# Performance work log

Measured on AMD Instinct MI355X. Metric: run time of the kernel, lower is better.

The kernel has to match this reference:

```python
import jax, jax.numpy as jnp
import numpy as np

B, T, D, I, C, H = 8192, 128, 7, 128, 10, 64
L = 2 ** D
SUBSET = int(I * 0.8)  # feature_subset_size = 102


def setup_inputs() -> dict:
    key = jax.random.key(0)
    ks = jax.random.split(key, 7)
    x = jax.random.normal(ks[0], (B, I), dtype=jnp.float32)
    # exact feature-subset mask: SUBSET ones per (tree, depth) row
    r = jax.random.uniform(ks[1], (T, D, I))
    ranks = jnp.argsort(jnp.argsort(r, axis=-1), axis=-1)
    feature_mask = (ranks < SUBSET).astype(jnp.float32)
    thresholds = jax.random.normal(ks[2], (T, D), dtype=jnp.float32)
    leaf_outputs = jax.random.normal(ks[3], (T, L, C), dtype=jnp.float32)
    W1 = jax.random.normal(ks[4], (I, H), dtype=jnp.float32) * 0.08
    b1 = jnp.zeros((H,), dtype=jnp.float32)
    W2 = jax.random.normal(ks[5], (H, T), dtype=jnp.float32) * 0.12
    b2 = jnp.zeros((T,), dtype=jnp.float32)
    return {"x": x, "feature_mask": feature_mask, "thresholds": thresholds,
            "leaf_outputs": leaf_outputs, "W1": W1, "b1": b1, "W2": W2, "b2": b2}


def reference(x, feature_mask, thresholds, leaf_outputs, W1, b1, W2, b2):
    depth = thresholds.shape[1]
    # split logits: masked feature sum minus threshold, per (batch, tree, depth)
    z = jnp.einsum('bi,tdi->btd', x, feature_mask) - thresholds[None, :, :]
    s = 0.5 * (z / (1.0 + jnp.abs(z)) + 1.0)  # scaled softsign split in (0,1)
    # probabilistic path routing: doubling concat, identical to torch loop
    p = jnp.ones((x.shape[0], feature_mask.shape[0], 1), dtype=x.dtype)
    for d in range(depth):
        sd = s[:, :, d:d + 1]            # [B, T, 1]
        p = jnp.concatenate([p * sd, p * (1.0 - sd)], axis=-1)  # [B, T, 2^(d+1)]
    leaf_probs = jax.nn.softmax(leaf_outputs, axis=-1)           # [T, L, C]
    tree_outputs = jnp.einsum('btl,tlc->btc', p, leaf_probs)     # [B, T, C]
    # instance-wise attention over trees (eval mode: no dropout)
    attn = jax.nn.softmax(jax.nn.relu(x @ W1 + b1) @ W2 + b2, axis=-1)  # [B, T]
    return jnp.sum(tree_outputs * attn[:, :, None], axis=1)     # [B, C]
```

## Files before the change

kernel.cpp:

```cpp
#include <hip/hip_runtime.h>
#include <hip/hip_bf16.h>
#include <hip/hip_fp16.h>


#define BB 8192
#define TT 128
#define II 128
#define CC 10
#define HH 64

#define OFF_LPB 524288
#define OFF_XBF 606208
#define OFF_MBF 1130496

typedef __attribute__((ext_vector_type(8))) short short8;
typedef __attribute__((ext_vector_type(16))) float floatx16;

static __device__ inline unsigned int pkbf(float lo, float hi) {
  __hip_bfloat162 h = __float22bfloat162_rn(make_float2(lo, hi));
  unsigned int u;
  __builtin_memcpy(&u, &h, 4);
  return u;
}

static __device__ inline unsigned int pkh(float lo, float hi) {
  __half2 h = __float22half2_rn(make_float2(lo, hi));
  unsigned int u;
  __builtin_memcpy(&u, &h, 4);
  return u;
}

static __device__ inline short8 cvt8(float4 a, float4 b) {
  union { short8 v; unsigned int u[4]; } r;
  r.u[0] = pkbf(a.x, a.y);
  r.u[1] = pkbf(a.z, a.w);
  r.u[2] = pkbf(b.x, b.y);
  r.u[3] = pkbf(b.z, b.w);
  return r.v;
}

__global__ __launch_bounds__(64) void prep_kernel(
    const float* __restrict__ x, const float* __restrict__ mask,
    const float* __restrict__ lo,
    const float* __restrict__ W1, const float* __restrict__ b1,
    const float* __restrict__ W2, const float* __restrict__ b2,
    __half* __restrict__ attnB, unsigned int* __restrict__ lpbG,
    unsigned short* __restrict__ xbf, unsigned short* __restrict__ mbf,
    float* __restrict__ out) {
  __shared__ __align__(16) char smem_raw[6144];
  const int blk = blockIdx.x;
  const int lane = threadIdx.x;
  const int half = lane >> 5, l31 = lane & 31;

  if (blk < 256) {
    const int b0 = blk * 32;

    short8 axf[8];
    const float* xrow = x + (size_t)(b0 + l31) * II + half * 8;
#pragma unroll
    for (int s = 0; s < 8; ++s)
      axf[s] = cvt8(*(const float4*)(xrow + s * 16),
                    *(const float4*)(xrow + s * 16 + 4));

    floatx16 acch[2];
#pragma unroll
    for (int i = 0; i < 16; ++i) { acch[0][i] = 0.f; acch[1][i] = 0.f; }
#pragma unroll
    for (int s = 0; s < 8; ++s) {
#pragma unroll
      for (int tile = 0; tile < 2; ++tile) {
        union { short8 v; unsigned int u[4]; } wf;
#pragma unroll
        for (int jp = 0; jp < 4; ++jp) {
          int k0 = s * 16 + half * 8 + jp * 2;
          float f0 = W1[(size_t)k0 * HH + tile * 32 + l31];
          float f1 = W1[(size_t)(k0 + 1) * HH + tile * 32 + l31];
          wf.u[jp] = pkbf(f0, f1);
        }
        acch[tile] = __builtin_amdgcn_mfma_f32_32x32x16_bf16(
            axf[s], wf.v, acch[tile], 0, 0, 0);
      }
    }
    __hip_bfloat16* hids = (__hip_bfloat16*)smem_raw;
#pragma unroll
    for (int tile = 0; tile < 2; ++tile) {
      float bh = b1[tile * 32 + l31];
#pragma unroll
      for (int r = 0; r < 16; ++r) {
        int row = (r & 3) + 8 * (r >> 2) + 4 * half;
        hids[row * 72 + tile * 32 + l31] =
            __float2bfloat16(fmaxf(acch[tile][r] + bh, 0.f));
      }
    }
    __syncthreads();

    short8 ahf[4];
#pragma unroll
    for (int s = 0; s < 4; ++s)
      ahf[s] = *(const short8*)(hids + l31 * 72 + s * 16 + half * 8);

    floatx16 accl[4];
#pragma unroll
    for (int tile = 0; tile < 4; ++tile) {
#pragma unroll
      for (int i = 0; i < 16; ++i) accl[tile][i] = 0.f;
#pragma unroll
      for (int s = 0; s < 4; ++s) {
        union { short8 v; unsigned int u[4]; } wf;
#pragma unroll
        for (int jp = 0; jp < 4; ++jp) {
          int k0 = s * 16 + half * 8 + jp * 2;
          float f0 = W2[(size_t)k0 * TT + tile * 32 + l31];
          float f1 = W2[(size_t)(k0 + 1) * TT + tile * 32 + l31];
          wf.u[jp] = pkbf(f0, f1);
        }
        accl[tile] = __builtin_amdgcn_mfma_f32_32x32x16_bf16(
            ahf[s], wf.v, accl[tile], 0, 0, 0);
      }
      float bt = b2[tile * 32 + l31];
#pragma unroll
      for (int i = 0; i < 16; ++i) accl[tile][i] += bt;
    }

    float mrow[16];
#pragma unroll
    for (int r = 0; r < 16; ++r)
      mrow[r] = fmaxf(fmaxf(accl[0][r], accl[1][r]),
                      fmaxf(accl[2][r], accl[3][r]));
#pragma unroll
    for (int msk = 1; msk <= 16; msk <<= 1)
#pragma unroll
      for (int r = 0; r < 16; ++r)
        mrow[r] = fmaxf(mrow[r], __shfl_xor(mrow[r], msk, 64));
    float srow[16];
#pragma unroll
    for (int r = 0; r < 16; ++r) srow[r] = 0.f;
#pragma unroll
    for (int tile = 0; tile < 4; ++tile)
#pragma unroll
      for (int r = 0; r < 16; ++r) {
        float e = __expf(accl[tile][r] - mrow[r]);
        accl[tile][r] = e;
        srow[r] += e;
      }
#pragma unroll
    for (int msk = 1; msk <= 16; msk <<= 1)
#pragma unroll
      for (int r = 0; r < 16; ++r)
        srow[r] += __shfl_xor(srow[r], msk, 64);
#pragma unroll
    for (int r = 0; r < 16; ++r) srow[r] = 1.f / srow[r];

#pragma unroll
    for (int tile = 0; tile < 4; ++tile)
#pragma unroll
      for (int r = 0; r < 16; ++r) {
        int row = (r & 3) + 8 * (r >> 2) + 4 * half;
        attnB[(size_t)(b0 + row) * TT + tile * 32 + l31] =
            __float2half(accl[tile][r] * srow[r]);
      }

  } else if (blk < 384) {
    float* lps = (float*)smem_raw;
    const int t0 = blk - 256;
#pragma unroll
    for (int rr = 0; rr < 2; ++rr) {
      int l = lane * 2 + rr;
      const float* row = lo + ((size_t)t0 * 128 + l) * CC;
      float v[CC];
      float m = -1e30f;
#pragma unroll
      for (int c = 0; c < CC; ++c) { v[c] = row[c]; m = fmaxf(m, v[c]); }
      float s = 0.f;
#pragma unroll
      for (int c = 0; c < CC; ++c) { v[c] = __expf(v[c] - m); s += v[c]; }
      float inv = 1.f / s;
      float* o = lps + l * 12;
#pragma unroll
      for (int c = 0; c < CC; ++c) o[c] = v[c] * inv;
    }
    __syncthreads();

#pragma unroll
    for (int jj = 0; jj < 3; ++jj) {
      int idx = jj * 64 + lane;
      if (idx < 160) {
        int s = idx / 20, e = idx - s * 20;
        int n = e >> 1, hf = e & 1;
        unsigned int wd[4];
#pragma unroll
        for (int jp = 0; jp < 4; ++jp) {
          int l0 = s * 16 + hf * 8 + jp * 2;
          float f0 = lps[l0 * 12 + n];
          float f1 = lps[(l0 + 1) * 12 + n];
          wd[jp] = pkh(f0, f1);
        }
        ((uint4*)lpbG)[(size_t)t0 * 160 + idx] =
            make_uint4(wd[0], wd[1], wd[2], wd[3]);
      }
    }
  } else if (blk < 668) {
    const float* src;
    unsigned short* dst;
    size_t base;
    if (blk < 640) { src = x;    dst = xbf; base = (size_t)(blk - 384) * 4096; }
    else           { src = mask; dst = mbf; base = (size_t)(blk - 640) * 4096; }
#pragma unroll
    for (int j = 0; j < 8; ++j) {
      size_t e = base + (size_t)j * 512 + (size_t)lane * 8;
      float4 a = *(const float4*)(src + e);
      float4 b = *(const float4*)(src + e + 4);
      *(short8*)(dst + e) = cvt8(a, b);
    }
  } else {
    const int base4 = (blk - 668) * 512;
#pragma unroll
    for (int j = 0; j < 8; ++j)
      ((float4*)out)[base4 + j * 64 + lane] = make_float4(0.f, 0.f, 0.f, 0.f);
  }
}

__global__ __launch_bounds__(256, 4) void main_kernel(
    const unsigned short* __restrict__ xbf, const unsigned short* __restrict__ mbf,
    const float* __restrict__ thr, const __half* __restrict__ attnB,
    const unsigned int* __restrict__ lpbG, float* __restrict__ out) {
  __shared__ __align__(16) char smem_raw[16384];
  const int tid = threadIdx.x;
  const int wv = tid >> 6, lane = tid & 63;
  const int half = lane >> 5, l31 = lane & 31;
  const int phys = blockIdx.x;
  const int bg2 = (phys & 7) + ((phys >> 7) << 3);
  const int tg  = (phys >> 3) & 15;
  const int bl = wv * 32 + l31;

  __half* zsl = (__half*)smem_raw;

  __half av[8];
  *(uint4*)av = ((const uint4*)attnB)[(size_t)(bg2 * 128 + bl) * 16 + tg];

  {
    const int m0 = tg * 56;
    short8 xf[8];
    const unsigned short* xr = xbf + (size_t)(bg2 * 128 + bl) * II + half * 8;
#pragma unroll
    for (int s = 0; s < 8; ++s) xf[s] = *(const short8*)(xr + s * 16);

#pragma unroll
    for (int tile = 0; tile < 2; ++tile) {
      int mr = m0 + tile * 28 + l31; if (mr > 895) mr = 895;
      const unsigned short* mrow = mbf + (size_t)mr * II + half * 8;
      short8 af[8];
#pragma unroll
      for (int s = 0; s < 8; ++s) af[s] = *(const short8*)(mrow + s * 16);
      float th[16];
#pragma unroll
      for (int r = 0; r < 16; ++r) {
        int row = (r & 3) + 8 * (r >> 2) + 4 * half;
        int mrr = m0 + tile * 28 + row;
        th[r] = thr[mrr > 895 ? 895 : mrr];
      }
      floatx16 acc;
#pragma unroll
      for (int i = 0; i < 16; ++i) acc[i] = 0.f;
#pragma unroll
      for (int s = 0; s < 8; ++s)
        acc = __builtin_amdgcn_mfma_f32_32x32x16_bf16(af[s], xf[s], acc, 0, 0, 0);

#pragma unroll
      for (int r = 0; r < 16; ++r) {
        int row = (r & 3) + 8 * (r >> 2) + 4 * half;
        if (row < 28) {
          int tl = row / 7;
          int d = row - tl * 7;
          float z = acc[r] - th[r];
          float o = 0.5f * (z / (1.f + fabsf(z)) + 1.f);
          zsl[((tl + tile * 4) * 128 + bl) * 8 + d] = __float2half(o);
        }
      }
    }
  }

  {
    const uint4* zsl4 = (const uint4*)smem_raw;
    const uint4* lpt = (const uint4*)lpbG + (size_t)tg * 1280;

    floatx16 acc;
#pragma unroll
    for (int i = 0; i < 16; ++i) acc[i] = 0.f;

    auto dostep = [&](int it, const uint4* bf) {
      uint4 sv = zsl4[it * 128 + bl];
      const __half* sh = (const __half*)&sv;
      float s0 = __half2float(sh[0]), s1 = __half2float(sh[1]);
      float s2 = __half2float(sh[2]), s3 = __half2float(sh[3]);
      float s4 = __half2float(sh[4]), s5 = __half2float(sh[5]);
      float s6 = __half2float(sh[6]);
      float A  = __half2float(av[it]);

      float s0c = 1.f - s0, s1c = 1.f - s1, s2c = 1.f - s2;
      float t0 = s0 * s1, t1 = s0c * s1, t2 = s0 * s1c, t3 = s0c * s1c;
      float pl[8];
      pl[0] = t0 * s2;  pl[1] = t1 * s2;  pl[2] = t2 * s2;  pl[3] = t3 * s2;
      pl[4] = t0 * s2c; pl[5] = t1 * s2c; pl[6] = t2 * s2c; pl[7] = t3 * s2c;
      float sel3 = half ? (1.f - s3) : s3;
      float Af = A * sel3;
      float s4c = 1.f - s4, s5c = 1.f - s5;
      float as6 = Af * s6, as6c = Af * (1.f - s6);
      float u0 = s4 * s5, u1 = s4c * s5, u2 = s4 * s5c, u3 = s4c * s5c;
      float wv8[8];
      wv8[0] = u0 * as6;  wv8[1] = u1 * as6;
      wv8[2] = u2 * as6;  wv8[3] = u3 * as6;
      wv8[4] = u0 * as6c; wv8[5] = u1 * as6c;
      wv8[6] = u2 * as6c; wv8[7] = u3 * as6c;
      __half2 pl2[4];
#pragma unroll
      for (int jp = 0; jp < 4; ++jp)
        pl2[jp] = __float22half2_rn(make_float2(pl[jp * 2], pl[jp * 2 + 1]));

#pragma unroll
      for (int s = 0; s < 8; ++s) {
        union { short8 v; __half2 h[4]; } a0;
        __half2 w2 = __half2half2(__float2half(wv8[s]));
#pragma unroll
        for (int jp = 0; jp < 4; ++jp) a0.h[jp] = __hmul2(pl2[jp], w2);
        acc = __builtin_amdgcn_mfma_f32_32x32x16_f16(
            a0.v, *(const short8*)&bf[s], acc, 0, 0, 0);
      }
    };

#define PF(dst, itn)                                                       \
  _Pragma("unroll") for (int s = 0; s < 8; ++s)                            \
      dst[s] = (l31 < CC) ? lpt[((itn) * 8 + s) * 20 + l31 * 2 + half]     \
                          : make_uint4(0u, 0u, 0u, 0u);

    uint4 bf0[8], bf1[8];
    PF(bf0, 0)
#pragma unroll
    for (int ith = 0; ith < 4; ++ith) {
      const int it = ith * 2;
      PF(bf1, it + 1)
      dostep(it, bf0);
      if (ith < 3) { PF(bf0, it + 2) }
      dostep(it + 1, bf1);
    }
#undef PF

    __syncthreads();
    float* red = (float*)smem_raw;
    if (l31 < CC) {
#pragma unroll
      for (int r = 0; r < 16; ++r) {
        int row = (r & 3) + 8 * (r >> 2) + 4 * half;
        red[(wv * 32 + row) * 10 + l31] = acc[r];
      }
    }
    __syncthreads();
#pragma unroll
    for (int j = 0; j < 5; ++j) {
      int idx = tid + 256 * j;
      atomicAdd(out + (size_t)bg2 * 1280 + idx, red[idx]);
    }
  }
}

extern "C" void kernel_launch(void* const* d_in, const int* in_sizes, int n_in,
                              void* d_out, int out_size, void* d_ws, size_t ws_size,
                              hipStream_t stream) {
  const float* x    = (const float*)d_in[0];
  const float* mask = (const float*)d_in[1];
  const float* thr  = (const float*)d_in[2];
  const float* lo   = (const float*)d_in[3];
  const float* W1   = (const float*)d_in[4];
  const float* b1   = (const float*)d_in[5];
  const float* W2   = (const float*)d_in[6];
  const float* b2   = (const float*)d_in[7];
  float* out = (float*)d_out;
  float* ws  = (float*)d_ws;

  __half*         attnB = (__half*)ws;
  unsigned int*   LPb   = (unsigned int*)(ws + OFF_LPB);
  unsigned short* xbf   = (unsigned short*)(ws + OFF_XBF);
  unsigned short* mbf   = (unsigned short*)(ws + OFF_MBF);

  prep_kernel<<<708, 64, 0, stream>>>(x, mask, lo, W1, b1, W2, b2,
                                      attnB, LPb, xbf, mbf, out);
  main_kernel<<<1024, 256, 0, stream>>>(xbf, mbf, thr, attnB, LPb, out);
}
```

Measured before the change: 101.7 us.

## Halve trees per block, stage leaf probs in LDS, double grid size

```diff
diff --git a/kernel.cpp b/kernel.cpp
--- a/kernel.cpp
+++ b/kernel.cpp
@@ -220,76 +220,84 @@
   }
 }
 
-__global__ __launch_bounds__(256, 4) void main_kernel(
+__global__ __launch_bounds__(256, 6) void main_kernel(
     const unsigned short* __restrict__ xbf, const unsigned short* __restrict__ mbf,
     const float* __restrict__ thr, const __half* __restrict__ attnB,
     const unsigned int* __restrict__ lpbG, float* __restrict__ out) {
-  __shared__ __align__(16) char smem_raw[16384];
+  __shared__ __align__(16) char smem_raw[18432];
   const int tid = threadIdx.x;
   const int wv = tid >> 6, lane = tid & 63;
   const int half = lane >> 5, l31 = lane & 31;
   const int phys = blockIdx.x;
-  const int bg2 = (phys & 7) + ((phys >> 7) << 3);
-  const int tg  = (phys >> 3) & 15;
+  const int bg2 = (phys & 7) * 8 + (phys >> 8);
+  const int tg4 = (phys >> 3) & 31;
   const int bl = wv * 32 + l31;
 
   __half* zsl = (__half*)smem_raw;
-
-  __half av[8];
-  *(uint4*)av = ((const uint4*)attnB)[(size_t)(bg2 * 128 + bl) * 16 + tg];
+  uint4* st4 = (uint4*)(smem_raw + 8192);
+
+  const uint4* lpg = (const uint4*)lpbG + (size_t)tg4 * 640;
+  uint4 stg0 = lpg[wv * 64 + lane];
+  uint4 stg1 = lpg[(wv + 4) * 64 + lane];
+  uint4 stg2 = make_uint4(0u, 0u, 0u, 0u);
+  if (wv < 2) stg2 = lpg[(wv + 8) * 64 + lane];
+
+  __half av[4];
+  *(uint2*)av = ((const uint2*)attnB)[(size_t)(bg2 * 128 + bl) * 32 + tg4];
 
   {
-    const int m0 = tg * 56;
+    const int m0 = tg4 * 28;
     short8 xf[8];
     const unsigned short* xr = xbf + (size_t)(bg2 * 128 + bl) * II + half * 8;
 #pragma unroll
     for (int s = 0; s < 8; ++s) xf[s] = *(const short8*)(xr + s * 16);
 
-#pragma unroll
-    for (int tile = 0; tile < 2; ++tile) {
-      int mr = m0 + tile * 28 + l31; if (mr > 895) mr = 895;
-      const unsigned short* mrow = mbf + (size_t)mr * II + half * 8;
-      short8 af[8];
-#pragma unroll
-      for (int s = 0; s < 8; ++s) af[s] = *(const short8*)(mrow + s * 16);
-      float th[16];
-#pragma unroll
-      for (int r = 0; r < 16; ++r) {
-        int row = (r & 3) + 8 * (r >> 2) + 4 * half;
-        int mrr = m0 + tile * 28 + row;
-        th[r] = thr[mrr > 895 ? 895 : mrr];
-      }
-      floatx16 acc;
-#pragma unroll
-      for (int i = 0; i < 16; ++i) acc[i] = 0.f;
-#pragma unroll
-      for (int s = 0; s < 8; ++s)
-        acc = __builtin_amdgcn_mfma_f32_32x32x16_bf16(af[s], xf[s], acc, 0, 0, 0);
-
-#pragma unroll
-      for (int r = 0; r < 16; ++r) {
-        int row = (r & 3) + 8 * (r >> 2) + 4 * half;
-        if (row < 28) {
-          int tl = row / 7;
-          int d = row - tl * 7;
-          float z = acc[r] - th[r];
-          float o = 0.5f * (z / (1.f + fabsf(z)) + 1.f);
-          zsl[((tl + tile * 4) * 128 + bl) * 8 + d] = __float2half(o);
-        }
+    int mr = m0 + l31; if (mr > 895) mr = 895;
+    const unsigned short* mrow = mbf + (size_t)mr * II + half * 8;
+
+    floatx16 acc;
+#pragma unroll
+    for (int i = 0; i < 16; ++i) acc[i] = 0.f;
+#pragma unroll
+    for (int s = 0; s < 8; ++s) {
+      short8 af = *(const short8*)(mrow + s * 16);
+      acc = __builtin_amdgcn_mfma_f32_32x32x16_bf16(af, xf[s], acc, 0, 0, 0);
+    }
+
+#pragma unroll
+    for (int r = 0; r < 16; ++r) {
+      int row = (r & 3) + 8 * (r >> 2) + 4 * half;
+      if (row < 28) {
+        int tl = row / 7;
+        int d = row - tl * 7;
+        float z = acc[r] - thr[m0 + row];
+        float o = 0.5f * (z / (1.f + fabsf(z)) + 1.f);
+        zsl[((tl * 128) + bl) * 8 + d] = __float2half(o);
       }
     }
   }
+
+  st4[wv * 64 + lane] = stg0;
+  st4[(wv + 4) * 64 + lane] = stg1;
+  if (wv < 2) st4[(wv + 8) * 64 + lane] = stg2;
+  __syncthreads();
 
   {
     const uint4* zsl4 = (const uint4*)smem_raw;
-    const uint4* lpt = (const uint4*)lpbG + (size_t)tg * 1280;
 
     floatx16 acc;
 #pragma unroll
     for (int i = 0; i < 16; ++i) acc[i] = 0.f;
 
-    auto dostep = [&](int it, const uint4* bf) {
+#pragma unroll
+    for (int it = 0; it < 4; ++it) {
+      uint4 bf[8];
+#pragma unroll
+      for (int s = 0; s < 8; ++s)
+        bf[s] = (l31 < CC) ? st4[(it * 8 + s) * 20 + l31 * 2 + half]
+                           : make_uint4(0u, 0u, 0u, 0u);
       uint4 sv = zsl4[it * 128 + bl];
+
       const __half* sh = (const __half*)&sv;
       float s0 = __half2float(sh[0]), s1 = __half2float(sh[1]);
       float s2 = __half2float(sh[2]), s3 = __half2float(sh[3]);
@@ -326,24 +334,7 @@
         acc = __builtin_amdgcn_mfma_f32_32x32x16_f16(
             a0.v, *(const short8*)&bf[s], acc, 0, 0, 0);
       }
-    };
-
-#define PF(dst, itn)                                                       \
-  _Pragma("unroll") for (int s = 0; s < 8; ++s)                            \
-      dst[s] = (l31 < CC) ? lpt[((itn) * 8 + s) * 20 + l31 * 2 + half]     \
-                          : make_uint4(0u, 0u, 0u, 0u);
-
-    uint4 bf0[8], bf1[8];
-    PF(bf0, 0)
-#pragma unroll
-    for (int ith = 0; ith < 4; ++ith) {
-      const int it = ith * 2;
-      PF(bf1, it + 1)
-      dostep(it, bf0);
-      if (ith < 3) { PF(bf0, it + 2) }
-      dostep(it + 1, bf1);
-    }
-#undef PF
+    }
 
     __syncthreads();
     float* red = (float*)smem_raw;
@@ -384,5 +375,5 @@
 
   prep_kernel<<<708, 64, 0, stream>>>(x, mask, lo, W1, b1, W2, b2,
                                       attnB, LPb, xbf, mbf, out);
-  main_kernel<<<1024, 256, 0, stream>>>(xbf, mbf, thr, attnB, LPb, out);
-}
+  main_kernel<<<2048, 256, 0, stream>>>(xbf, mbf, thr, attnB, LPb, out);
+}
```

After: 106.7 us. 1.05x slower.

## Keep split probabilities in registers via cross-half shuffles instead of LDS staging

Applied to the files above, without the earlier changes.

```diff
diff --git a/kernel.cpp b/kernel.cpp
--- a/kernel.cpp
+++ b/kernel.cpp
@@ -224,7 +224,7 @@
     const unsigned short* __restrict__ xbf, const unsigned short* __restrict__ mbf,
     const float* __restrict__ thr, const __half* __restrict__ attnB,
     const unsigned int* __restrict__ lpbG, float* __restrict__ out) {
-  __shared__ __align__(16) char smem_raw[16384];
+  __shared__ __align__(16) float red[1280];
   const int tid = threadIdx.x;
   const int wv = tid >> 6, lane = tid & 63;
   const int half = lane >> 5, l31 = lane & 31;
@@ -233,11 +233,10 @@
   const int tg  = (phys >> 3) & 15;
   const int bl = wv * 32 + l31;
 
-  __half* zsl = (__half*)smem_raw;
-
   __half av[8];
   *(uint4*)av = ((const uint4*)attnB)[(size_t)(bg2 * 128 + bl) * 16 + tg];
 
+  uint4 sv[8];
   {
     const int m0 = tg * 56;
     short8 xf[8];
@@ -249,53 +248,59 @@
     for (int tile = 0; tile < 2; ++tile) {
       int mr = m0 + tile * 28 + l31; if (mr > 895) mr = 895;
       const unsigned short* mrow = mbf + (size_t)mr * II + half * 8;
-      short8 af[8];
-#pragma unroll
-      for (int s = 0; s < 8; ++s) af[s] = *(const short8*)(mrow + s * 16);
-      float th[16];
+
+      floatx16 acc;
+#pragma unroll
+      for (int i = 0; i < 16; ++i) acc[i] = 0.f;
+#pragma unroll
+      for (int s = 0; s < 8; ++s) {
+        short8 af = *(const short8*)(mrow + s * 16);
+        acc = __builtin_amdgcn_mfma_f32_32x32x16_bf16(af, xf[s], acc, 0, 0, 0);
+      }
+
+      float o[16], po[16];
 #pragma unroll
       for (int r = 0; r < 16; ++r) {
         int row = (r & 3) + 8 * (r >> 2) + 4 * half;
         int mrr = m0 + tile * 28 + row;
-        th[r] = thr[mrr > 895 ? 895 : mrr];
-      }
-      floatx16 acc;
-#pragma unroll
-      for (int i = 0; i < 16; ++i) acc[i] = 0.f;
-#pragma unroll
-      for (int s = 0; s < 8; ++s)
-        acc = __builtin_amdgcn_mfma_f32_32x32x16_bf16(af[s], xf[s], acc, 0, 0, 0);
-
-#pragma unroll
-      for (int r = 0; r < 16; ++r) {
-        int row = (r & 3) + 8 * (r >> 2) + 4 * half;
-        if (row < 28) {
-          int tl = row / 7;
-          int d = row - tl * 7;
-          float z = acc[r] - th[r];
-          float o = 0.5f * (z / (1.f + fabsf(z)) + 1.f);
-          zsl[((tl + tile * 4) * 128 + bl) * 8 + d] = __float2half(o);
-        }
-      }
+        float th = thr[mrr > 895 ? 895 : mrr];
+        float z = acc[r] - th;
+        o[r] = 0.5f * (z / (1.f + fabsf(z)) + 1.f);
+      }
+#pragma unroll
+      for (int r = 0; r < 16; ++r) po[r] = __shfl_xor(o[r], 32, 64);
+      float lo16[16], hi16[16];
+#pragma unroll
+      for (int r = 0; r < 16; ++r) {
+        lo16[r] = half ? po[r] : o[r];
+        hi16[r] = half ? o[r] : po[r];
+      }
+#define OA(rw) (((((rw) >> 2) & 1) ? hi16 : lo16)[((rw) & 3) + (((rw) >> 3) << 2)])
+#pragma unroll
+      for (int tl = 0; tl < 4; ++tl) {
+        sv[tile * 4 + tl] = make_uint4(
+            pkh(OA(7 * tl + 0), OA(7 * tl + 1)),
+            pkh(OA(7 * tl + 2), OA(7 * tl + 3)),
+            pkh(OA(7 * tl + 4), OA(7 * tl + 5)),
+            pkh(OA(7 * tl + 6), OA(7 * tl + 6)));
+      }
+#undef OA
     }
   }
 
   {
-    const uint4* zsl4 = (const uint4*)smem_raw;
     const uint4* lpt = (const uint4*)lpbG + (size_t)tg * 1280;
 
     floatx16 acc;
 #pragma unroll
     for (int i = 0; i < 16; ++i) acc[i] = 0.f;
 
-    auto dostep = [&](int it, const uint4* bf) {
-      uint4 sv = zsl4[it * 128 + bl];
-      const __half* sh = (const __half*)&sv;
+    auto dostep = [&](int it, const uint4* bf, uint4 svv, float A) {
+      const __half* sh = (const __half*)&svv;
       float s0 = __half2float(sh[0]), s1 = __half2float(sh[1]);
       float s2 = __half2float(sh[2]), s3 = __half2float(sh[3]);
       float s4 = __half2float(sh[4]), s5 = __half2float(sh[5]);
       float s6 = __half2float(sh[6]);
-      float A  = __half2float(av[it]);
 
       float s0c = 1.f - s0, s1c = 1.f - s1, s2c = 1.f - s2;
       float t0 = s0 * s1, t1 = s0c * s1, t2 = s0 * s1c, t3 = s0c * s1c;
@@ -339,14 +344,12 @@
     for (int ith = 0; ith < 4; ++ith) {
       const int it = ith * 2;
       PF(bf1, it + 1)
-      dostep(it, bf0);
+      dostep(it, bf0, sv[it], __half2float(av[it]));
       if (ith < 3) { PF(bf0, it + 2) }
-      dostep(it + 1, bf1);
+      dostep(it + 1, bf1, sv[it + 1], __half2float(av[it + 1]));
     }
 #undef PF
 
-    __syncthreads();
-    float* red = (float*)smem_raw;
     if (l31 < CC) {
 #pragma unroll
       for (int r = 0; r < 16; ++r) {
```

After: 110.2 us. 8.4% more time.
